# Kernel optimization log

Hardware: AMD Instinct MI355X
Metric: run time of the kernel (lower is better)

The kernel has to match this reference:

```python
import jax, jax.numpy as jnp
import numpy as np

COST_CLASS, COST_BBOX, COST_GIOU = 1.0, 5.0, 2.0


def _to_xyxy(b):
    cx, cy, w, h = b[..., 0], b[..., 1], b[..., 2], b[..., 3]
    return jnp.stack([cx - w / 2, cy - h / 2, cx + w / 2, cy + h / 2], axis=-1)


def _generalized_box_iou(a, b):
    # a: [N,4] xyxy, b: [M,4] xyxy -> [N,M]
    area_a = (a[:, 2] - a[:, 0]) * (a[:, 3] - a[:, 1])
    area_b = (b[:, 2] - b[:, 0]) * (b[:, 3] - b[:, 1])
    lt = jnp.maximum(a[:, None, :2], b[None, :, :2])
    rb = jnp.minimum(a[:, None, 2:], b[None, :, 2:])
    wh = jnp.clip(rb - lt, 0.0)
    inter = wh[..., 0] * wh[..., 1]
    union = area_a[:, None] + area_b[None, :] - inter
    iou = inter / union
    lt_c = jnp.minimum(a[:, None, :2], b[None, :, :2])
    rb_c = jnp.maximum(a[:, None, 2:], b[None, :, 2:])
    wh_c = jnp.clip(rb_c - lt_c, 0.0)
    area_c = wh_c[..., 0] * wh_c[..., 1]
    return iou - (area_c - union) / area_c


@jax.jit
def _cost_matrix(class_probs, pred_boxes, tgt_boxes, tgt_labels):
    bs, q, k = class_probs.shape
    probs_flat = class_probs.reshape(bs * q, k)
    cost_class = -probs_flat[:, tgt_labels]                          # [BQ, T]
    cost_bbox = jnp.abs(pred_boxes.reshape(bs * q, 1, 4) - tgt_boxes[None, :, :]).sum(-1)
    cost_giou = -_generalized_box_iou(_to_xyxy(pred_boxes.reshape(bs * q, 4)), _to_xyxy(tgt_boxes))
    C = COST_BBOX * cost_bbox + COST_CLASS * cost_class + COST_GIOU * cost_giou
    return C.reshape(bs, q, -1)


def _hungarian(cost):
    # min-cost assignment, cost [n, m] with n <= m (e-maxx JV algorithm).
    n, m = cost.shape
    INF = 1e18
    u = np.zeros(n + 1)
    v = np.zeros(m + 1)
    p = np.zeros(m + 1, dtype=np.int64)
    way = np.zeros(m + 1, dtype=np.int64)
    for i in range(1, n + 1):
        p[0] = i
        j0 = 0
        minv = np.full(m + 1, INF)
        used = np.zeros(m + 1, dtype=bool)
        while True:
            used[j0] = True
            i0 = p[j0]
            cj = cost[i0 - 1] - u[i0] - v[1:]
            upd = (~used[1:]) & (cj < minv[1:])
            minv[1:] = np.where(upd, cj, minv[1:])
            way[1:] = np.where(upd, j0, way[1:])
            free_vals = np.where(used[1:], INF, minv[1:])
            j1 = int(np.argmin(free_vals)) + 1
            delta = free_vals[j1 - 1]
            used_idx = np.nonzero(used)[0]
            u[p[used_idx]] += delta
            v[used_idx] -= delta
            minv[1:] = np.where(used[1:], minv[1:], minv[1:] - delta)
            j0 = j1
            if p[j0] == 0:
                break
        while j0:
            j1 = way[j0]
            p[j0] = p[j1]
            j0 = j1
    rows = p[1:] - 1                      # for each col: matched row or -1
    cols = np.nonzero(rows >= 0)[0]
    return rows[cols], cols               # (row_idx per match, col_idx) sorted by col


def setup_inputs() -> dict:
    key = jax.random.key(0)
    k1, k2, k3, k4 = jax.random.split(key, 4)
    bs, q, k, t_total = 64, 300, 91, 4096
    class_probs = jax.random.uniform(k1, (bs, q, k), dtype=jnp.float32)
    pred_boxes = jax.random.uniform(k2, (bs, q, 4), dtype=jnp.float32)
    tgt_boxes = jax.random.uniform(k3, (t_total, 4), dtype=jnp.float32)
    tgt_labels = jax.random.randint(k4, (t_total,), 0, k)
    return {"class_probs": class_probs, "pred_boxes": pred_boxes,
            "tgt_boxes": tgt_boxes, "tgt_labels": tgt_labels}


def reference(class_probs, pred_boxes, tgt_boxes, tgt_labels):
    bs, q, _ = class_probs.shape
    t_per = tgt_boxes.shape[0] // bs      # equal #targets per image
    C = _cost_matrix(class_probs, pred_boxes, tgt_boxes, tgt_labels)
    C_np = np.asarray(C)
    pred_idx, tgt_idx = [], []
    for b in range(bs):                   # per-batch assignment, as in the original
        c = C_np[b][:, b * t_per:(b + 1) * t_per]      # [Q, T], Q > T
        t_rows, q_cols = _hungarian(c.T)               # assign each target a query
        pred_idx.append(q_cols)
        tgt_idx.append(t_rows)
    return C, jnp.asarray(np.stack(pred_idx)), jnp.asarray(np.stack(tgt_idx))
```

## Files before the change

kernel.cpp:

```cpp
#include <hip/hip_runtime.h>

#define BS   64
#define Q    300
#define K    91
#define T    4096
#define TPER 64
#define M    300
#define NR   64
#define WS_STRIDE 304

__device__ __forceinline__ float cost_entry(const float4 pb, const float4 tb,
                                            const float prob)
{
    const float px0 = pb.x - pb.z * 0.5f, py0 = pb.y - pb.w * 0.5f;
    const float px1 = pb.x + pb.z * 0.5f, py1 = pb.y + pb.w * 0.5f;
    const float parea = (px1 - px0) * (py1 - py0);
    const float tx0 = tb.x - tb.z * 0.5f, ty0 = tb.y - tb.w * 0.5f;
    const float tx1 = tb.x + tb.z * 0.5f, ty1 = tb.y + tb.w * 0.5f;
    const float tarea = (tx1 - tx0) * (ty1 - ty0);
    const float bb = fabsf(pb.x - tb.x) + fabsf(pb.y - tb.y)
                   + fabsf(pb.z - tb.z) + fabsf(pb.w - tb.w);
    const float iw = fmaxf(fminf(px1, tx1) - fmaxf(px0, tx0), 0.f);
    const float ih = fmaxf(fminf(py1, ty1) - fmaxf(py0, ty0), 0.f);
    const float inter = iw * ih;
    const float uni   = parea + tarea - inter;
    const float iou   = inter * __builtin_amdgcn_rcpf(uni);
    const float cw  = fmaxf(fmaxf(px1, tx1) - fminf(px0, tx0), 0.f);
    const float ch  = fmaxf(fmaxf(py1, ty1) - fminf(py0, ty0), 0.f);
    const float carea = cw * ch;
    const float giou  = iou - (carea - uni) * __builtin_amdgcn_rcpf(carea);
    return 5.0f * bb - prob - 2.0f * giou;
}

__device__ void cost_block(int cb, const float* __restrict__ probs,
                           const float* __restrict__ pboxes,
                           const float* __restrict__ tboxes,
                           const int* __restrict__ tlabels,
                           float* __restrict__ C)
{
    __shared__ float sprobs[4][K];
    const int tid = threadIdx.x;
    const int bq0 = cb * 4;
    for (int idx = tid; idx < 4 * K; idx += 64)
        sprobs[idx / K][idx % K] = probs[(size_t)bq0 * K + idx];
    float4 pbr[4];
#pragma unroll
    for (int r = 0; r < 4; ++r) pbr[r] = ((const float4*)pboxes)[bq0 + r];
    __syncthreads();

#pragma unroll 1
    for (int c = 0; c < 16; ++c) {
        const int t0 = (c << 8) + (tid << 2);
        const int4 lb4 = *(const int4*)(tlabels + t0);
        float out[4][4];
#pragma unroll
        for (int k = 0; k < 4; ++k) {
            const float4 tb = ((const float4*)tboxes)[t0 + k];
            const int lab = (k == 0) ? lb4.x : (k == 1) ? lb4.y : (k == 2) ? lb4.z : lb4.w;
#pragma unroll
            for (int r = 0; r < 4; ++r)
                out[r][k] = cost_entry(pbr[r], tb, sprobs[r][lab]);
        }
#pragma unroll
        for (int r = 0; r < 4; ++r)
            *(float4*)&C[(size_t)(bq0 + r) * T + t0] =
                make_float4(out[r][0], out[r][1], out[r][2], out[r][3]);
    }
}

__device__ void hungarian_block(int b, const float* __restrict__ probs,
                                const float* __restrict__ pboxes,
                                const float* __restrict__ tboxes,
                                const int* __restrict__ tlabels,
                                float* __restrict__ wslice,
                                float* __restrict__ pred_out,
                                float* __restrict__ tgt_out)
{
    __shared__ int p[M + 1];
    __shared__ int way[M + 1];
    const int tid = threadIdx.x;
    const bool lv = (tid < 60);
    const int c0 = lv ? 5 * tid : 0;

    float4 pbx[5];
#pragma unroll
    for (int s = 0; s < 5; ++s)
        pbx[s] = ((const float4*)pboxes)[b * Q + c0 + s];
#pragma unroll 1
    for (int i = 0; i < NR; ++i) {
        const float4 tb = ((const float4*)tboxes)[b * TPER + i];
        const int lab = tlabels[b * TPER + i];
        const size_t pbase = (size_t)(b * Q + c0) * K + lab;
#pragma unroll
        for (int s = 0; s < 5; ++s) {
            const float pr = probs[pbase + (size_t)s * K];
            const float val = cost_entry(pbx[s], tb, pr);
            if (lv) wslice[i * WS_STRIDE + c0 + s] = val;
        }
    }

    double u_reg = 0.0;
    double v_[5], minv_[5];
#pragma unroll
    for (int s = 0; s < 5; ++s) v_[s] = 0.0;
    const unsigned used0 = lv ? 0u : 0x1fu;
    for (int j = tid; j <= M; j += 64) p[j] = 0;
    __syncthreads();

#pragma unroll 1
    for (int i = 1; i <= NR; ++i) {
        if (tid == 0) p[0] = i;
        unsigned usedmask = used0;
        bool inTree = false;
#pragma unroll
        for (int s = 0; s < 5; ++s) minv_[s] = 1e18;
        int i0 = i, j0 = 0;
        float crow[5];
        {
            const float* rp = wslice + (size_t)(i0 - 1) * WS_STRIDE + c0;
#pragma unroll
            for (int s = 0; s < 5; ++s) crow[s] = rp[s];
        }
        int guard = 0;
        while (true) {
            if (tid == i0 - 1) inTree = true;
            const double ui0 = __shfl(u_reg, i0 - 1);
            double lmin = 1e18; int lidx = 0x7fffffff;
#pragma unroll
            for (int s = 0; s < 5; ++s) {
                if (!((usedmask >> s) & 1u)) {
                    const double cj = (double)crow[s] - ui0 - v_[s];
                    if (cj < minv_[s]) { minv_[s] = cj; way[c0 + s + 1] = j0; }
                    if (minv_[s] < lmin) { lmin = minv_[s]; lidx = c0 + s; }
                }
            }
            double rv = lmin; int ri = lidx;
#pragma unroll
            for (int off = 32; off > 0; off >>= 1) {
                const double ov = __shfl_xor(rv, off);
                const int    oi = __shfl_xor(ri, off);
                if (ov < rv || (ov == rv && oi < ri)) { rv = ov; ri = oi; }
            }
            const double delta = rv;
            const int c1 = ri, j1 = c1 + 1;
            const int i0n = p[j1];
            float crow2[5];
            if (i0n) {
                const float* rp2 = wslice + (size_t)(i0n - 1) * WS_STRIDE + c0;
#pragma unroll
                for (int s = 0; s < 5; ++s) crow2[s] = rp2[s];
            }
            if (inTree) u_reg += delta;
#pragma unroll
            for (int s = 0; s < 5; ++s) {
                if ((usedmask >> s) & 1u) v_[s] -= delta;
                else                      minv_[s] -= delta;
            }
            if (lv && c1 >= c0 && c1 < c0 + 5) usedmask |= 1u << (c1 - c0);
            j0 = j1;
            if (!i0n || ++guard > 128) break;
            i0 = i0n;
#pragma unroll
            for (int s = 0; s < 5; ++s) crow[s] = crow2[s];
        }
        __syncthreads();
        if (tid == 0) {
            int jj = j0;
            while (jj) { const int jn = way[jj]; p[jj] = p[jn]; jj = jn; }
        }
        __syncthreads();
    }

    int cnt = 0;
#pragma unroll
    for (int s = 0; s < 5; ++s)
        if (lv && p[c0 + s + 1] > 0) ++cnt;
    int incl = cnt;
#pragma unroll
    for (int off = 1; off < 64; off <<= 1) {
        const int t = __shfl_up(incl, off);
        if (tid >= off) incl += t;
    }
    int pos = incl - cnt;
#pragma unroll
    for (int s = 0; s < 5; ++s) {
        if (lv) {
            const int pi = p[c0 + s + 1];
            if (pi > 0) {
                pred_out[b * TPER + pos] = (float)(c0 + s);
                tgt_out [b * TPER + pos] = (float)(pi - 1);
                ++pos;
            }
        }
    }
}

__global__ __launch_bounds__(64) void fused_kernel(
    const float* __restrict__ probs, const float* __restrict__ pboxes,
    const float* __restrict__ tboxes, const int* __restrict__ tlabels,
    float* __restrict__ C, float* __restrict__ pred_out,
    float* __restrict__ tgt_out, float* __restrict__ ws)
{
    const int bid = blockIdx.x;
    if (bid < BS)
        hungarian_block(bid, probs, pboxes, tboxes, tlabels,
                        ws + (size_t)bid * NR * WS_STRIDE, pred_out, tgt_out);
    else
        cost_block(bid - BS, probs, pboxes, tboxes, tlabels, C);
}

__global__ __launch_bounds__(256) void cost_kernel_fb(
    const float* __restrict__ probs, const float* __restrict__ pboxes,
    const float* __restrict__ tboxes, const int* __restrict__ tlabels,
    float* __restrict__ C)
{
    __shared__ float sprobs[4][K];
    const int tid = threadIdx.x;
    const int bq0 = blockIdx.x * 4;
    for (int idx = tid; idx < 4 * K; idx += 256)
        sprobs[idx / K][idx % K] = probs[(size_t)bq0 * K + idx];
    float4 pbr[4];
#pragma unroll
    for (int r = 0; r < 4; ++r) pbr[r] = ((const float4*)pboxes)[bq0 + r];
    __syncthreads();
#pragma unroll
    for (int c = 0; c < 4; ++c) {
        const int t0 = (c << 10) + (tid << 2);
        const int4 lb4 = *(const int4*)(tlabels + t0);
        float out[4][4];
#pragma unroll
        for (int k = 0; k < 4; ++k) {
            const float4 tb = ((const float4*)tboxes)[t0 + k];
            const int lab = (k == 0) ? lb4.x : (k == 1) ? lb4.y : (k == 2) ? lb4.z : lb4.w;
#pragma unroll
            for (int r = 0; r < 4; ++r)
                out[r][k] = cost_entry(pbr[r], tb, sprobs[r][lab]);
        }
#pragma unroll
        for (int r = 0; r < 4; ++r)
            *(float4*)&C[(size_t)(bq0 + r) * T + t0] =
                make_float4(out[r][0], out[r][1], out[r][2], out[r][3]);
    }
}

__global__ __launch_bounds__(64) void hungarian_kernel_fb(
    const float* __restrict__ C, float* __restrict__ pred_out,
    float* __restrict__ tgt_out)
{
    __shared__ float  cost[NR * M];
    __shared__ double v[M + 1], minv[M + 1], u[NR + 1];
    __shared__ int    p[M + 1], way[M + 1];
    __shared__ unsigned char used[M + 1];
    const int b = blockIdx.x;
    const int tid = threadIdx.x;
    const double INF = 1e18;
    for (int e = tid; e < NR * M; e += 64) {
        const int q = e >> 6, i = e & 63;
        cost[i * M + q] = C[(size_t)b * Q * T + (size_t)q * T + b * TPER + i];
    }
    for (int j = tid; j <= M; j += 64) { v[j] = 0.0; p[j] = 0; }
    for (int j = tid; j <= NR; j += 64) u[j] = 0.0;
    __syncthreads();
    for (int i = 1; i <= NR; ++i) {
        if (tid == 0) p[0] = i;
        for (int j = tid; j <= M; j += 64) { minv[j] = INF; used[j] = 0; }
        __syncthreads();
        int j0 = 0;
        while (true) {
            if (tid == 0) used[j0] = 1;
            __syncthreads();
            const int    i0  = p[j0];
            const double ui0 = u[i0];
            const float* crow = &cost[(i0 - 1) * M];
            double lmin = INF; int lidx = M + 1;
            for (int j = tid + 1; j <= M; j += 64) {
                if (!used[j]) {
                    double mv = minv[j];
                    const double cj = (double)crow[j - 1] - ui0 - v[j];
                    if (cj < mv) { mv = cj; minv[j] = cj; way[j] = j0; }
                    if (mv < lmin) { lmin = mv; lidx = j; }
                }
            }
#pragma unroll
            for (int off = 32; off > 0; off >>= 1) {
                const double oval = __shfl_down(lmin, off);
                const int    oidx = __shfl_down(lidx, off);
                if (oval < lmin || (oval == lmin && oidx < lidx)) { lmin = oval; lidx = oidx; }
            }
            const int    j1    = __shfl(lidx, 0);
            const double delta = __shfl(lmin, 0);
            __syncthreads();
            for (int j = tid; j <= M; j += 64) {
                if (used[j]) { u[p[j]] += delta; v[j] -= delta; }
                else          minv[j] -= delta;
            }
            __syncthreads();
            j0 = j1;
            if (p[j0] == 0) break;
        }
        if (tid == 0) {
            int jj = j0;
            while (jj) { const int j1 = way[jj]; p[jj] = p[j1]; jj = j1; }
        }
        __syncthreads();
    }
    if (tid == 0) {
        int kk = 0;
        for (int j = 1; j <= M; ++j) {
            if (p[j] > 0) {
                pred_out[b * TPER + kk] = (float)(j - 1);
                tgt_out [b * TPER + kk] = (float)(p[j] - 1);
                ++kk;
            }
        }
    }
}

extern "C" void kernel_launch(void* const* d_in, const int* in_sizes, int n_in,
                              void* d_out, int out_size, void* d_ws, size_t ws_size,
                              hipStream_t stream) {
    const float* probs   = (const float*)d_in[0];
    const float* pboxes  = (const float*)d_in[1];
    const float* tboxes  = (const float*)d_in[2];
    const int*   tlabels = (const int*)  d_in[3];

    float* C    = (float*)d_out;
    float* pred = C + (size_t)BS * Q * T;
    float* tgt  = pred + (size_t)BS * TPER;

    const size_t ws_needed = (size_t)BS * NR * WS_STRIDE * sizeof(float);
    if (ws_size >= ws_needed) {
        hipLaunchKernelGGL(fused_kernel, dim3(BS + BS * Q / 4), dim3(64), 0, stream,
                           probs, pboxes, tboxes, tlabels, C, pred, tgt, (float*)d_ws);
    } else {
        hipLaunchKernelGGL(cost_kernel_fb, dim3(BS * Q / 4), dim3(256), 0, stream,
                           probs, pboxes, tboxes, tlabels, C);
        hipLaunchKernelGGL(hungarian_kernel_fb, dim3(BS), dim3(64), 0, stream,
                           C, pred, tgt);
    }
}
```

Baseline: 445.6 us.

## Warm-start Hungarian with row-minimum duals and greedy matching; prefetch cost-block inputs

The Hungarian solver now sets each row's dual to its minimum cost and greedily assigns each row to its argmin column when that column is free. Already-matched rows skip the augmenting-path search, so fewer sequential augmentations run. The cost-matrix block also transposes probabilities in shared memory for float4 reads, prefetches the next chunk of target boxes and labels, and uses nontemporal stores. The guard on path length is raised to 512 so that longer augmenting paths are not cut off. In exchange the warm start adds a serial greedy loop on one thread and changes the tie-breaking order, so the chosen assignment can differ from the reference when costs tie.

```diff
diff --git a/kernel.cpp b/kernel.cpp
--- a/kernel.cpp
+++ b/kernel.cpp
@@ -8,6 +8,8 @@
 #define M    300
 #define NR   64
 #define WS_STRIDE 304
+
+typedef float __attribute__((ext_vector_type(4))) f32x4;
 
 __device__ __forceinline__ float cost_entry(const float4 pb, const float4 tb,
                                             const float prob)
@@ -38,33 +40,64 @@
                            const int* __restrict__ tlabels,
                            float* __restrict__ C)
 {
-    __shared__ float sprobs[4][K];
+    __shared__ __align__(16) float sprob4[K][4];
     const int tid = threadIdx.x;
     const int bq0 = cb * 4;
-    for (int idx = tid; idx < 4 * K; idx += 64)
-        sprobs[idx / K][idx % K] = probs[(size_t)bq0 * K + idx];
+    for (int idx = tid; idx < 4 * K; idx += 64) {
+        const int k = idx >> 2, r = idx & 3;
+        sprob4[k][r] = probs[(size_t)(bq0 + r) * K + k];
+    }
     float4 pbr[4];
 #pragma unroll
     for (int r = 0; r < 4; ++r) pbr[r] = ((const float4*)pboxes)[bq0 + r];
     __syncthreads();
 
+    const float4* tbv = (const float4*)tboxes;
+    const int4*   lbv = (const int4*)tlabels;
+
+    int4 lb = lbv[tid];
+    float4 tb[4];
+#pragma unroll
+    for (int k = 0; k < 4; ++k) tb[k] = tbv[(tid << 2) + k];
+
 #pragma unroll 1
     for (int c = 0; c < 16; ++c) {
+        int4 lbn = {0, 0, 0, 0};
+        float4 tbn[4];
+        if (c < 15) {
+            const int nt0 = ((c + 1) << 8) + (tid << 2);
+            lbn = lbv[nt0 >> 2];
+#pragma unroll
+            for (int k = 0; k < 4; ++k) tbn[k] = tbv[nt0 + k];
+        }
+        const int labs[4] = { lb.x, lb.y, lb.z, lb.w };
+        float4 pr[4];
+#pragma unroll
+        for (int k = 0; k < 4; ++k)
+            pr[k] = *(const float4*)sprob4[labs[k]];
+
         const int t0 = (c << 8) + (tid << 2);
-        const int4 lb4 = *(const int4*)(tlabels + t0);
         float out[4][4];
 #pragma unroll
         for (int k = 0; k < 4; ++k) {
-            const float4 tb = ((const float4*)tboxes)[t0 + k];
-            const int lab = (k == 0) ? lb4.x : (k == 1) ? lb4.y : (k == 2) ? lb4.z : lb4.w;
-#pragma unroll
-            for (int r = 0; r < 4; ++r)
-                out[r][k] = cost_entry(pbr[r], tb, sprobs[r][lab]);
-        }
-#pragma unroll
-        for (int r = 0; r < 4; ++r)
-            *(float4*)&C[(size_t)(bq0 + r) * T + t0] =
-                make_float4(out[r][0], out[r][1], out[r][2], out[r][3]);
+#pragma unroll
+            for (int r = 0; r < 4; ++r) {
+                const float prk = (r == 0) ? pr[k].x : (r == 1) ? pr[k].y
+                                : (r == 2) ? pr[k].z : pr[k].w;
+                out[r][k] = cost_entry(pbr[r], tb[k], prk);
+            }
+        }
+#pragma unroll
+        for (int r = 0; r < 4; ++r) {
+            f32x4 v = { out[r][0], out[r][1], out[r][2], out[r][3] };
+            __builtin_nontemporal_store(
+                v, (f32x4*)&C[(size_t)(bq0 + r) * T + t0]);
+        }
+        if (c < 15) {
+            lb = lbn;
+#pragma unroll
+            for (int k = 0; k < 4; ++k) tb[k] = tbn[k];
+        }
     }
 }
 
@@ -78,6 +111,7 @@
 {
     __shared__ int p[M + 1];
     __shared__ int way[M + 1];
+    __shared__ int rargArr[NR];
     const int tid = threadIdx.x;
     const bool lv = (tid < 60);
     const int c0 = lv ? 5 * tid : 0;
@@ -86,29 +120,60 @@
 #pragma unroll
     for (int s = 0; s < 5; ++s)
         pbx[s] = ((const float4*)pboxes)[b * Q + c0 + s];
+
+    float rmin_f = 1e30f; int rarg = 0;
 #pragma unroll 1
     for (int i = 0; i < NR; ++i) {
         const float4 tb = ((const float4*)tboxes)[b * TPER + i];
         const int lab = tlabels[b * TPER + i];
         const size_t pbase = (size_t)(b * Q + c0) * K + lab;
+        float vals[5];
+        float lmin = 1e30f; int lidx = 0x7fffffff;
 #pragma unroll
         for (int s = 0; s < 5; ++s) {
             const float pr = probs[pbase + (size_t)s * K];
-            const float val = cost_entry(pbx[s], tb, pr);
-            if (lv) wslice[i * WS_STRIDE + c0 + s] = val;
-        }
-    }
-
-    double u_reg = 0.0;
+            vals[s] = cost_entry(pbx[s], tb, pr);
+            if (lv && vals[s] < lmin) { lmin = vals[s]; lidx = c0 + s; }
+        }
+        if (lv) {
+#pragma unroll
+            for (int s = 0; s < 5; ++s)
+                wslice[i * WS_STRIDE + c0 + s] = vals[s];
+        }
+        float rv = lv ? lmin : 1e30f; int ri = lidx;
+#pragma unroll
+        for (int off = 32; off > 0; off >>= 1) {
+            const float ov = __shfl_xor(rv, off);
+            const int   oi = __shfl_xor(ri, off);
+            if (ov < rv || (ov == rv && oi < ri)) { rv = ov; ri = oi; }
+        }
+        if (tid == i) { rmin_f = rv; rarg = ri; }
+    }
+    double u_reg = (double)rmin_f;
+
+    rargArr[tid] = rarg;
+    for (int j = tid; j <= M; j += 64) p[j] = 0;
+    __syncthreads();
+
+    unsigned long long m0 = 0ull;
+    if (tid == 0) {
+#pragma unroll 1
+        for (int r = 0; r < NR; ++r) {
+            const int ac = rargArr[r] + 1;
+            if (p[ac] == 0) { p[ac] = r + 1; m0 |= 1ull << r; }
+        }
+    }
+    __syncthreads();
+    const unsigned long long matchedRows = __shfl(m0, 0);
+
     double v_[5], minv_[5];
 #pragma unroll
     for (int s = 0; s < 5; ++s) v_[s] = 0.0;
     const unsigned used0 = lv ? 0u : 0x1fu;
-    for (int j = tid; j <= M; j += 64) p[j] = 0;
-    __syncthreads();
 
 #pragma unroll 1
     for (int i = 1; i <= NR; ++i) {
+        if ((matchedRows >> (i - 1)) & 1ull) continue;
         if (tid == 0) p[0] = i;
         unsigned usedmask = used0;
         bool inTree = false;
@@ -158,7 +223,7 @@
             }
             if (lv && c1 >= c0 && c1 < c0 + 5) usedmask |= 1u << (c1 - c0);
             j0 = j1;
-            if (!i0n || ++guard > 128) break;
+            if (!i0n || ++guard > 512) break;
             i0 = i0n;
 #pragma unroll
             for (int s = 0; s < 5; ++s) crow[s] = crow2[s];
```

After: 410.9 us. 7.8% less time.
